# Kernel optimization log

Measured on AMD Instinct MI355X. Metric: run time of the kernel, lower is better.

The kernel has to match this reference:

```python
import jax, jax.numpy as jnp
import numpy as np

EPS = 1e-5

def _conv1x1(x, w, b):
    # x: [B, Cin, L], w: [Cout, Cin], b: [Cout]
    return jnp.einsum('oc,bcl->bol', w, x) + b[None, :, None]

def _bn(x, g, b):
    # BatchNorm1d in training mode: batch stats over (B, L), biased variance
    m = jnp.mean(x, axis=(0, 2), keepdims=True)
    v = jnp.var(x, axis=(0, 2), keepdims=True)
    return g[None, :, None] * (x - m) * jax.lax.rsqrt(v + EPS) + b[None, :, None]

def setup_inputs() -> dict:
    key = jax.random.key(0)
    ks = jax.random.split(key, 16)
    B, H, L, K = 32, 32, 32768, 7
    rel, im, out = H // 16, H // 8, H // 4          # 2, 4, 8
    cat = (1 + K) * rel                              # 16
    w = lambda k, shape: jax.random.normal(k, shape, jnp.float32) * 0.1
    return {
        'x': jax.random.normal(ks[0], (B, H, L), jnp.float32),
        'w_phi': w(ks[1], (rel, H)),  'b_phi': w(ks[2], (rel,)),
        'w_psi': w(ks[3], (rel, H)),  'b_psi': w(ks[4], (rel,)),
        'w_beta': w(ks[5], (out, H)), 'b_beta': w(ks[6], (out,)),
        'w_cw1': w(ks[7], (im, cat)), 'b_cw1': w(ks[8], (im,)),
        'w_cw2': w(ks[9], (out, im)), 'b_cw2': w(ks[10], (out,)),
        'w_out': w(ks[11], (H, out)), 'b_out': w(ks[12], (H,)),
        'g_cat': jnp.ones((cat,), jnp.float32),  'be_cat': jnp.zeros((cat,), jnp.float32),
        'g_im': jnp.ones((im,), jnp.float32),    'be_im': jnp.zeros((im,), jnp.float32),
        'g_aggr': jnp.ones((out,), jnp.float32), 'be_aggr': jnp.zeros((out,), jnp.float32),
        'g_hid': jnp.ones((H,), jnp.float32),    'be_hid': jnp.zeros((H,), jnp.float32),
        'kernel_size': 7,
    }

def reference(x, w_phi, b_phi, w_psi, b_psi, w_beta, b_beta,
              w_cw1, b_cw1, w_cw2, b_cw2, w_out, b_out,
              g_cat, be_cat, g_im, be_im, g_aggr, be_aggr, g_hid, be_hid,
              kernel_size):
    B, H, L = x.shape
    phi = _conv1x1(x, w_phi, b_phi)                       # [B, rel, L]
    psi = _conv1x1(x, w_psi, b_psi)                       # [B, rel, L]
    p = kernel_size // 2
    psi_pad = jnp.pad(psi, ((0, 0), (0, 0), (p, p)))
    # F.unfold with kernel (k,1): channel index = c*k + j -> stack kernel axis after channel
    psi_unf = jnp.stack([psi_pad[:, :, j:j + L] for j in range(kernel_size)], axis=2)
    psi_unf = psi_unf.reshape(B, psi.shape[1] * kernel_size, L)   # [B, rel*k, L]
    h = jnp.concatenate([phi, psi_unf], axis=1)           # [B, (1+k)*rel, L]
    h = jax.nn.relu(_bn(h, g_cat, be_cat))
    h = _conv1x1(h, w_cw1, b_cw1)
    h = jax.nn.relu(_bn(h, g_im, be_im))
    weight = _conv1x1(h, w_cw2, b_cw2)                    # [B, out, L]
    beta = _conv1x1(x, w_beta, b_beta)                    # [B, out, L]
    aggr = jax.nn.relu(_bn(weight * beta, g_aggr, be_aggr))
    y = x + _conv1x1(aggr, w_out, b_out)
    return jax.nn.relu(_bn(y, g_hid, be_hid))
```

## Files before the change

### kernel.cpp

```cpp
#include <hip/hip_runtime.h>
#include <math.h>

#define Bn 32
#define Hc 32
#define Ln 32768
#define RELC 2
#define IMC 4
#define OC 8
#define CATC 16
#define KS 7
#define NPOS (Bn*Ln)
#define TPB 256
#define VPT 4
#define PPB (TPB*VPT)
#define TILES (Ln/PPB)
#define NBLK (Bn*TILES)
#define NSLOT 16
#define SSTR 128
#define PCH (RELC*PPB)
#define BCH (OC*PPB)
#define XCH (Hc*PPB)

#define iS_PHI  0
#define iSS_PHI 2
#define iS_PSI  4
#define iSS_PSI 6
#define iS_T    8
#define iSS_T   12
#define iS_AP   16
#define iSS_AP  24
#define iS_Y    32
#define iSS_Y   64
#define bPF  0
#define bPFS 6
#define bQL  12
#define bQLS 18
#define NBST 24

#define FMA4(A,S,V) { A.x=fmaf((S),(V).x,A.x); A.y=fmaf((S),(V).y,A.y); A.z=fmaf((S),(V).z,A.z); A.w=fmaf((S),(V).w,A.w); }

__device__ inline float4 affrelu(float4 v, float a, float d){
    float4 r;
    r.x=fmaxf(fmaf(a,v.x,d),0.f); r.y=fmaxf(fmaf(a,v.y,d),0.f);
    r.z=fmaxf(fmaf(a,v.z,d),0.f); r.w=fmaxf(fmaf(a,v.w,d),0.f);
    return r;
}
__device__ inline double wredd(double v){
    #pragma unroll
    for (int o=32;o>0;o>>=1) v += __shfl_down(v,o,64);
    return v;
}
__device__ inline float wredf(float v){
    #pragma unroll
    for (int o=32;o>0;o>>=1) v += __shfl_down(v,o,64);
    return v;
}
__device__ inline void atomAddD(double* p, double v){ unsafeAtomicAdd(p, v); }

__device__ inline unsigned short f2b(float f){
    unsigned int u = __float_as_uint(f);
    u += 0x7FFFu + ((u>>16)&1u);
    return (unsigned short)(u>>16);
}
__device__ inline float b2f(unsigned short h){ return __uint_as_float(((unsigned int)h)<<16); }
__device__ inline ushort4 pack4r(float4 v, float4* r){
    ushort4 h;
    h.x=f2b(v.x); h.y=f2b(v.y); h.z=f2b(v.z); h.w=f2b(v.w);
    r->x=b2f(h.x); r->y=b2f(h.y); r->z=b2f(h.z); r->w=b2f(h.w);
    return h;
}
__device__ inline ushort4 pack4(float4 v){
    ushort4 h;
    h.x=f2b(v.x); h.y=f2b(v.y); h.z=f2b(v.z); h.w=f2b(v.w);
    return h;
}
__device__ inline float4 unpack4(ushort4 h){
    return make_float4(b2f(h.x),b2f(h.y),b2f(h.z),b2f(h.w));
}
typedef unsigned short us8 __attribute__((ext_vector_type(8)));
typedef float f4nt __attribute__((ext_vector_type(4)));
__device__ inline void ntstore4(float* p, float4 v){
    union { float4 a; f4nt b; } u; u.a = v;
    __builtin_nontemporal_store(u.b, (f4nt*)p);
}

template<int NCH>
__device__ void affines(const double* __restrict__ stats, const double* __restrict__ bstats,
                        const float* g_cat, const float* be_cat,
                        const float* g_im,  const float* be_im,
                        const float* g_ag,  const float* be_ag,
                        const float* g_hid, const float* be_hid,
                        double (*redS)[16], double (*redQ)[16],
                        double* bstL, float* aAll, float* dAll, int tid)
{
    if (tid < NBST) bstL[tid] = bstats[tid];
    for (int p = tid; p < NCH*16; p += TPB){
        int ch = p >> 4, s = p & 15;
        int si, qi;
        if (ch < 2)       { si = iS_PHI+ch;           qi = iSS_PHI+ch; }
        else if (ch < 16) { int cp=(ch-2)/KS;         si = iS_PSI+cp;  qi = iSS_PSI+cp; }
        else if (ch < 20) { int i=ch-16;              si = iS_T+i;     qi = iSS_T+i; }
        else if (ch < 28) { int o=ch-20;              si = iS_AP+o;    qi = iSS_AP+o; }
        else              { int h=ch-28;              si = iS_Y+h;     qi = iSS_Y+h; }
        redS[ch][s] = stats[(size_t)s*SSTR + si];
        redQ[ch][s] = stats[(size_t)s*SSTR + qi];
    }
    __syncthreads();
    if (tid < NCH){
        double S=0, SS=0;
        #pragma unroll
        for (int s=0;s<16;++s){ S += redS[tid][s]; SS += redQ[tid][s]; }
        float g, be;
        if (tid < 16){
            if (tid >= 2){
                int cp=(tid-2)/KS, j=(tid-2)%KS, d=j-KS/2;
                if (d>0) for (int i=0;i<d;++i)   { S-=bstL[bPF+cp*3+i]; SS-=bstL[bPFS+cp*3+i]; }
                if (d<0) for (int i=3+d;i<3;++i) { S-=bstL[bQL+cp*3+i]; SS-=bstL[bQLS+cp*3+i]; }
            }
            g=g_cat[tid]; be=be_cat[tid];
        } else if (tid < 20){ g=g_im[tid-16]; be=be_im[tid-16]; }
        else if (tid < 28){ g=g_ag[tid-20]; be=be_ag[tid-20]; }
        else { g=g_hid[tid-28]; be=be_hid[tid-28]; }
        const double N=(double)NPOS;
        double m=S/N, v=SS/N-m*m, inv=1.0/sqrt(v+1e-5);
        aAll[tid]=(float)(g*inv);
        dAll[tid]=be-(float)(m*inv*g);
    }
}

__global__ void __launch_bounds__(TPB) k0(const float* __restrict__ x, unsigned short* __restrict__ xC)
{
    const int r = blockIdx.x;
    const int b = r >> 5, h = r & 31;
    const float* src = x + (size_t)r*Ln;
    unsigned short* dstBase = xC + (size_t)b*TILES*XCH + (size_t)h*PPB + threadIdx.x*4;
    const float* s4 = src + threadIdx.x*4;
    #pragma unroll 4
    for (int t = 0; t < TILES; ++t){
        float4 v = *(const float4*)(s4 + (size_t)t*PPB);
        *(ushort4*)(dstBase + (size_t)t*XCH) = pack4(v);
    }
}

__global__ void __launch_bounds__(TPB) k1c(
    const unsigned short* __restrict__ xC,
    const float* __restrict__ w_phi, const float* __restrict__ b_phi,
    const float* __restrict__ w_psi, const float* __restrict__ b_psi,
    const float* __restrict__ w_beta,const float* __restrict__ b_beta,
    unsigned short* __restrict__ phiC, unsigned short* __restrict__ psiC,
    unsigned short* __restrict__ betaC,
    double* __restrict__ stats, double* __restrict__ bstats)
{
    __shared__ __align__(16) float wl[Hc*12 + 12];
    __shared__ double rbuf[4][8];
    const int tid = threadIdx.x;
    for (int i = tid; i < Hc*12; i += TPB) {
        int h = i/12, j = i%12;
        float v;
        if (j < 2)      v = w_phi[j*Hc + h];
        else if (j < 4) v = w_psi[(j-2)*Hc + h];
        else            v = w_beta[(j-4)*Hc + h];
        wl[h*12 + j] = v;
    }
    if (tid < 12)
        wl[Hc*12+tid] = (tid<2) ? b_phi[tid] : (tid<4) ? b_psi[tid-2] : b_beta[tid-4];
    __syncthreads();

    const int cidx = blockIdx.x;
    const int tile = cidx % TILES;
    const int li   = tid*VPT;
    double* st = stats + (size_t)(cidx & (NSLOT-1))*SSTR;

    float4 acc[12];
    #pragma unroll
    for (int j=0;j<12;++j){ float bb = wl[Hc*12+j]; acc[j]=make_float4(bb,bb,bb,bb); }

    const unsigned short* xb = xC + (size_t)cidx*XCH + li;
    #pragma unroll 8
    for (int h=0; h<Hc; ++h) {
        const float4 xv = unpack4(*(const ushort4*)(xb + (size_t)h*PPB));
        const float4 w0 = *(const float4*)(&wl[h*12+0]);
        const float4 w1 = *(const float4*)(&wl[h*12+4]);
        const float4 w2 = *(const float4*)(&wl[h*12+8]);
        FMA4(acc[0],w0.x,xv); FMA4(acc[1],w0.y,xv); FMA4(acc[2],w0.z,xv); FMA4(acc[3],w0.w,xv);
        FMA4(acc[4],w1.x,xv); FMA4(acc[5],w1.y,xv); FMA4(acc[6],w1.z,xv); FMA4(acc[7],w1.w,xv);
        FMA4(acc[8],w2.x,xv); FMA4(acc[9],w2.y,xv); FMA4(acc[10],w2.z,xv); FMA4(acc[11],w2.w,xv);
    }
    float4 rphi[2], rpsi[2];
    #pragma unroll
    for (int c=0;c<RELC;++c){
        ushort4 hp = pack4r(acc[c], &rphi[c]);
        *(ushort4*)(phiC + (size_t)cidx*PCH + c*PPB + li) = hp;
        ushort4 hq = pack4r(acc[2+c], &rpsi[c]);
        *(ushort4*)(psiC + (size_t)cidx*PCH + c*PPB + li) = hq;
    }
    #pragma unroll
    for (int o=0;o<OC;++o)
        *(ushort4*)(betaC + (size_t)cidx*BCH + o*PPB + li) = pack4(acc[4+o]);

    double vals[8];
    #pragma unroll
    for (int c=0;c<2;++c){
        float4 v = rphi[c];
        vals[c]   = (double)v.x+v.y+v.z+v.w;
        vals[2+c] = (double)v.x*v.x+(double)v.y*v.y+(double)v.z*v.z+(double)v.w*v.w;
        float4 u = rpsi[c];
        vals[4+c] = (double)u.x+u.y+u.z+u.w;
        vals[6+c] = (double)u.x*u.x+(double)u.y*u.y+(double)u.z*u.z+(double)u.w*u.w;
    }
    if (tile==0 || tile==TILES-1) {
        #pragma unroll
        for (int c=0;c<2;++c){
            const float pv[4] = {rpsi[c].x, rpsi[c].y, rpsi[c].z, rpsi[c].w};
            #pragma unroll
            for (int e=0;e<4;++e){
                int le = tile*PPB + li + e;
                if (le < 3) {
                    atomAddD(&bstats[bPF +c*3+le], (double)pv[e]);
                    atomAddD(&bstats[bPFS+c*3+le], (double)pv[e]*pv[e]);
                }
                if (le >= Ln-3) {
                    int i = le-(Ln-3);
                    atomAddD(&bstats[bQL +c*3+i], (double)pv[e]);
                    atomAddD(&bstats[bQLS+c*3+i], (double)pv[e]*pv[e]);
                }
            }
        }
    }
    const int lane=tid&63, wid=tid>>6;
    #pragma unroll
    for (int i=0;i<8;++i){ double r=wredd(vals[i]); if(lane==0) rbuf[wid][i]=r; }
    __syncthreads();
    if (tid<8) atomAddD(&st[iS_PHI+tid], rbuf[0][tid]+rbuf[1][tid]+rbuf[2][tid]+rbuf[3][tid]);
}

#define STAGE_PSI_V(psiT)                                                                  \
    {                                                                                      \
        int c_ = tid >> 7, k_ = tid & 127;                                                 \
        us8 v_ = *(const us8*)(psiC + (size_t)cidx*PCH + c_*PPB + 8*k_);                   \
        _Pragma("unroll")                                                                  \
        for (int j_=0;j_<8;++j_) psiT[c_][3+8*k_+j_] = b2f(v_[j_]);                        \
        if (tid < 6){ int cc=tid/3, ii=tid%3;                                              \
            psiT[cc][ii] = (tile>0) ? b2f(psiC[(size_t)(cidx-1)*PCH + cc*PPB + 1021+ii]) : 0.f; }\
        else if (tid < 12){ int kk=tid-6, cc=kk/3, ii=kk%3;                                \
            psiT[cc][1027+ii] = (tile<TILES-1) ? b2f(psiC[(size_t)(cidx+1)*PCH + cc*PPB + ii]) : 0.f; } \
    }

#define COMPUTE_T(tacc,aCat,dCat,w1s,b1s,psiT)                                             \
    _Pragma("unroll")                                                                      \
    for (int o=0;o<IMC;++o){ float bb=b1s[o]; tacc[o]=make_float4(bb,bb,bb,bb); }          \
    _Pragma("unroll")                                                                      \
    for (int c=0;c<RELC;++c){                                                              \
        float4 pv = unpack4(*(const ushort4*)(phiC + (size_t)cidx*PCH + c*PPB + li));      \
        float4 hv = affrelu(pv, aCat[c], dCat[c]);                                         \
        _Pragma("unroll")                                                                  \
        for (int o=0;o<IMC;++o) FMA4(tacc[o], w1s[o*CATC+c], hv);                          \
    }                                                                                      \
    _Pragma("unroll")                                                                      \
    for (int c=0;c<RELC;++c){                                                              \
        float4 A  = *(const float4*)&psiT[c][li];                                          \
        float4 Bv = *(const float4*)&psiT[c][li+4];                                        \
        float4 Cv = *(const float4*)&psiT[c][li+8];                                        \
        float pr[12] = {A.x,A.y,A.z,A.w, Bv.x,Bv.y,Bv.z,Bv.w, Cv.x,Cv.y,Cv.z,Cv.w};        \
        _Pragma("unroll")                                                                  \
        for (int j=0;j<KS;++j){                                                            \
            int ch = 2 + c*KS + j;                                                         \
            float a=aCat[ch], d=dCat[ch];                                                  \
            float4 hv;                                                                     \
            hv.x=fmaxf(fmaf(a,pr[j+0],d),0.f);                                             \
            hv.y=fmaxf(fmaf(a,pr[j+1],d),0.f);                                             \
            hv.z=fmaxf(fmaf(a,pr[j+2],d),0.f);                                             \
            hv.w=fmaxf(fmaf(a,pr[j+3],d),0.f);                                             \
            _Pragma("unroll")                                                              \
            for (int o=0;o<IMC;++o) FMA4(tacc[o], w1s[o*CATC+ch], hv);                     \
        }                                                                                  \
    }

#define COMPUTE_AG(ag,tacc,aIm,dIm,aAg,dAg,w2s,b2s)                                        \
    {                                                                                      \
        float4 h2[IMC];                                                                    \
        _Pragma("unroll")                                                                  \
        for (int i=0;i<IMC;++i) h2[i]=affrelu(tacc[i],aIm[i],dIm[i]);                      \
        _Pragma("unroll")                                                                  \
        for (int o=0;o<OC;++o){                                                            \
            float bb=b2s[o];                                                               \
            float4 w=make_float4(bb,bb,bb,bb);                                             \
            _Pragma("unroll")                                                              \
            for (int i=0;i<IMC;++i) FMA4(w,w2s[o*IMC+i],h2[i]);                            \
            float4 bv = unpack4(*(const ushort4*)(betaC + (size_t)cidx*BCH + o*PPB + li)); \
            float4 av; av.x=w.x*bv.x; av.y=w.y*bv.y; av.z=w.z*bv.z; av.w=w.w*bv.w;         \
            ag[o]=affrelu(av, aAg[o], dAg[o]);                                             \
        }                                                                                  \
    }

__global__ void __launch_bounds__(TPB) k3t(
    const unsigned short* __restrict__ phiC, const unsigned short* __restrict__ psiC,
    const float* __restrict__ w_cw1, const float* __restrict__ b_cw1,
    const float* __restrict__ g_cat, const float* __restrict__ be_cat,
    double* __restrict__ stats, const double* __restrict__ bstats)
{
    __shared__ float w1s[IMC*CATC], b1s[IMC];
    __shared__ __align__(16) float psiT[2][1032];
    __shared__ double rbuf[4][8];
    __shared__ double redS[16][16], redQ[16][16];
    __shared__ double bstL[NBST];
    __shared__ float aAll[16], dAll[16];
    const int tid = threadIdx.x;
    const int cidx = blockIdx.x;
    const int tile = cidx % TILES;
    const int li   = tid*VPT;
    double* st = stats + (size_t)(cidx & (NSLOT-1))*SSTR;

    if (tid < IMC*CATC) w1s[tid] = w_cw1[tid];
    if (tid < IMC)      b1s[tid] = b_cw1[tid];
    STAGE_PSI_V(psiT)
    affines<16>(stats,bstats, g_cat,be_cat, 0,0, 0,0, 0,0, redS,redQ,bstL,aAll,dAll, tid);
    __syncthreads();

    float4 tacc[IMC];
    COMPUTE_T(tacc,aAll,dAll,w1s,b1s,psiT)

    double vals[8];
    #pragma unroll
    for (int o=0;o<IMC;++o){
        float4 v = tacc[o];
        vals[o]   = (double)v.x+v.y+v.z+v.w;
        vals[4+o] = (double)v.x*v.x+(double)v.y*v.y+(double)v.z*v.z+(double)v.w*v.w;
    }
    const int lane=tid&63, wid=tid>>6;
    #pragma unroll
    for (int i=0;i<8;++i){ double r=wredd(vals[i]); if(lane==0) rbuf[wid][i]=r; }
    __syncthreads();
    if (tid<8) atomAddD(&st[iS_T+tid], rbuf[0][tid]+rbuf[1][tid]+rbuf[2][tid]+rbuf[3][tid]);
}

__global__ void __launch_bounds__(TPB) k5a(
    const unsigned short* __restrict__ phiC, const unsigned short* __restrict__ psiC,
    const unsigned short* __restrict__ betaC,
    const float* __restrict__ w_cw1, const float* __restrict__ b_cw1,
    const float* __restrict__ w_cw2, const float* __restrict__ b_cw2,
    const float* __restrict__ g_cat, const float* __restrict__ be_cat,
    const float* __restrict__ g_im,  const float* __restrict__ be_im,
    double* __restrict__ stats, const double* __restrict__ bstats)
{
    __shared__ float w1s[IMC*CATC], b1s[IMC], w2s[OC*IMC], b2s[OC];
    __shared__ __align__(16) float psiT[2][1032];
    __shared__ double rbuf[4][16];
    __shared__ double redS[20][16], redQ[20][16];
    __shared__ double bstL[NBST];
    __shared__ float aAll[20], dAll[20];
    const int tid = threadIdx.x;
    const int cidx = blockIdx.x;
    const int tile = cidx % TILES;
    const int li   = tid*VPT;
    double* st = stats + (size_t)(cidx & (NSLOT-1))*SSTR;

    if (tid < IMC*CATC) w1s[tid] = w_cw1[tid];
    if (tid < IMC)      b1s[tid] = b_cw1[tid];
    if (tid>=64 && tid<64+OC*IMC) w2s[tid-64]=w_cw2[tid-64];
    if (tid>=96 && tid<96+OC)     b2s[tid-96]=b_cw2[tid-96];
    STAGE_PSI_V(psiT)
    affines<20>(stats,bstats, g_cat,be_cat, g_im,be_im, 0,0, 0,0, redS,redQ,bstL,aAll,dAll, tid);
    __syncthreads();

    float4 tacc[IMC];
    COMPUTE_T(tacc,aAll,dAll,w1s,b1s,psiT)

    double vals[16];
    {
        float4 h2[IMC];
        #pragma unroll
        for (int i=0;i<IMC;++i) h2[i]=affrelu(tacc[i],aAll[16+i],dAll[16+i]);
        #pragma unroll
        for (int o=0;o<OC;++o){
            float bb=b2s[o];
            float4 w=make_float4(bb,bb,bb,bb);
            #pragma unroll
            for (int i=0;i<IMC;++i) FMA4(w,w2s[o*IMC+i],h2[i]);
            float4 bv = unpack4(*(const ushort4*)(betaC + (size_t)cidx*BCH + o*PPB + li));
            float4 av; av.x=w.x*bv.x; av.y=w.y*bv.y; av.z=w.z*bv.z; av.w=w.w*bv.w;
            vals[o]   = (double)av.x+av.y+av.z+av.w;
            vals[8+o] = (double)av.x*av.x+(double)av.y*av.y+(double)av.z*av.z+(double)av.w*av.w;
        }
    }
    const int lane=tid&63, wid=tid>>6;
    #pragma unroll
    for (int i=0;i<16;++i){ double r=wredd(vals[i]); if(lane==0) rbuf[wid][i]=r; }
    __syncthreads();
    if (tid<16) atomAddD(&st[iS_AP+tid], rbuf[0][tid]+rbuf[1][tid]+rbuf[2][tid]+rbuf[3][tid]);
}

__global__ void __launch_bounds__(TPB) k7y(
    const unsigned short* __restrict__ xC,
    const unsigned short* __restrict__ phiC, const unsigned short* __restrict__ psiC,
    const unsigned short* __restrict__ betaC,
    const float* __restrict__ w_cw1, const float* __restrict__ b_cw1,
    const float* __restrict__ w_cw2, const float* __restrict__ b_cw2,
    const float* __restrict__ w_out, const float* __restrict__ b_out,
    const float* __restrict__ g_cat, const float* __restrict__ be_cat,
    const float* __restrict__ g_im,  const float* __restrict__ be_im,
    const float* __restrict__ g_ag,  const float* __restrict__ be_ag,
    double* __restrict__ stats, const double* __restrict__ bstats)
{
    __shared__ float w1s[IMC*CATC], b1s[IMC], w2s[OC*IMC], b2s[OC];
    __shared__ __align__(16) float wos[Hc*OC];
    __shared__ float bos[Hc];
    __shared__ __align__(16) float psiT[2][1032];
    __shared__ float fredS[Hc][4], fredQ[Hc][4];
    __shared__ double redS[28][16], redQ[28][16];
    __shared__ double bstL[NBST];
    __shared__ float aAll[28], dAll[28];
    const int tid = threadIdx.x;
    const int cidx = blockIdx.x;
    const int tile = cidx % TILES;
    const int li   = tid*VPT;
    double* st = stats + (size_t)(cidx & (NSLOT-1))*SSTR;

    if (tid < IMC*CATC) w1s[tid] = w_cw1[tid];
    if (tid < IMC)      b1s[tid] = b_cw1[tid];
    if (tid>=64 && tid<64+OC*IMC) w2s[tid-64]=w_cw2[tid-64];
    if (tid>=96 && tid<96+OC)     b2s[tid-96]=b_cw2[tid-96];
    wos[tid] = w_out[tid];
    if (tid>=128 && tid<128+Hc) bos[tid-128]=b_out[tid-128];
    STAGE_PSI_V(psiT)
    affines<28>(stats,bstats, g_cat,be_cat, g_im,be_im, g_ag,be_ag, 0,0,
                redS,redQ,bstL,aAll,dAll, tid);
    __syncthreads();

    float4 tacc[IMC];
    COMPUTE_T(tacc,aAll,dAll,w1s,b1s,psiT)
    float4 ag[OC];
    COMPUTE_AG(ag,tacc,(aAll+16),(dAll+16),(aAll+20),(dAll+20),w2s,b2s)

    const int lane=tid&63, wid=tid>>6;
    const unsigned short* xb = xC + (size_t)cidx*XCH + li;
    #pragma unroll 8
    for (int h=0;h<Hc;++h){
        float4 y = unpack4(*(const ushort4*)(xb + (size_t)h*PPB));
        float bb=bos[h]; y.x+=bb; y.y+=bb; y.z+=bb; y.w+=bb;
        #pragma unroll
        for (int o=0;o<OC;++o) FMA4(y, wos[h*OC+o], ag[o]);
        float fs=y.x+y.y+y.z+y.w;
        float fq=y.x*y.x+y.y*y.y+y.z*y.z+y.w*y.w;
        fs=wredf(fs); fq=wredf(fq);
        if (lane==0){ fredS[h][wid]=fs; fredQ[h][wid]=fq; }
    }
    __syncthreads();
    if (tid<Hc){
        double s=(double)fredS[tid][0]+fredS[tid][1]+fredS[tid][2]+fredS[tid][3];
        double q=(double)fredQ[tid][0]+fredQ[tid][1]+fredQ[tid][2]+fredQ[tid][3];
        atomAddD(&st[iS_Y +tid], s);
        atomAddD(&st[iSS_Y+tid], q);
    }
}

__global__ void __launch_bounds__(TPB) k9o(
    const unsigned short* __restrict__ xC,
    const unsigned short* __restrict__ phiC, const unsigned short* __restrict__ psiC,
    const unsigned short* __restrict__ betaC,
    const float* __restrict__ w_cw1, const float* __restrict__ b_cw1,
    const float* __restrict__ w_cw2, const float* __restrict__ b_cw2,
    const float* __restrict__ w_out, const float* __restrict__ b_out,
    const float* __restrict__ g_cat, const float* __restrict__ be_cat,
    const float* __restrict__ g_im,  const float* __restrict__ be_im,
    const float* __restrict__ g_ag,  const float* __restrict__ be_ag,
    const float* __restrict__ g_hid, const float* __restrict__ be_hid,
    float* __restrict__ out,
    const double* __restrict__ stats, const double* __restrict__ bstats)
{
    __shared__ float w1s[IMC*CATC], b1s[IMC], w2s[OC*IMC], b2s[OC];
    __shared__ __align__(16) float wos[Hc*OC];
    __shared__ float bos[Hc];
    __shared__ __align__(16) float psiT[2][1032];
    __shared__ double redS[60][16], redQ[60][16];
    __shared__ double bstL[NBST];
    __shared__ float aAll[60], dAll[60];
    const int tid = threadIdx.x;
    const int cidx = blockIdx.x;
    const int b    = cidx / TILES;
    const int tile = cidx % TILES;
    const int li   = tid*VPT;

    if (tid < IMC*CATC) w1s[tid] = w_cw1[tid];
    if (tid < IMC)      b1s[tid] = b_cw1[tid];
    if (tid>=64 && tid<64+OC*IMC) w2s[tid-64]=w_cw2[tid-64];
    if (tid>=96 && tid<96+OC)     b2s[tid-96]=b_cw2[tid-96];
    wos[tid] = w_out[tid];
    if (tid>=128 && tid<128+Hc) bos[tid-128]=b_out[tid-128];
    STAGE_PSI_V(psiT)
    affines<60>(stats,bstats, g_cat,be_cat, g_im,be_im, g_ag,be_ag, g_hid,be_hid,
                redS,redQ,bstL,aAll,dAll, tid);
    __syncthreads();

    float4 tacc[IMC];
    COMPUTE_T(tacc,aAll,dAll,w1s,b1s,psiT)
    float4 ag[OC];
    COMPUTE_AG(ag,tacc,(aAll+16),(dAll+16),(aAll+20),(dAll+20),w2s,b2s)

    const unsigned short* xb = xC + (size_t)cidx*XCH + li;
    float* ob = out + (size_t)b*Hc*Ln + (size_t)tile*PPB + li;
    #pragma unroll 8
    for (int h=0;h<Hc;++h){
        float4 y = unpack4(*(const ushort4*)(xb + (size_t)h*PPB));
        float bb=bos[h]; y.x+=bb; y.y+=bb; y.z+=bb; y.w+=bb;
        #pragma unroll
        for (int o=0;o<OC;++o) FMA4(y, wos[h*OC+o], ag[o]);
        ntstore4(ob + (size_t)h*Ln, affrelu(y, aAll[28+h], dAll[28+h]));
    }
}

extern "C" void kernel_launch(void* const* d_in, const int* in_sizes, int n_in,
                              void* d_out, int out_size, void* d_ws, size_t ws_size,
                              hipStream_t stream)
{
    const float* x     =(const float*)d_in[0];
    const float* w_phi =(const float*)d_in[1];  const float* b_phi =(const float*)d_in[2];
    const float* w_psi =(const float*)d_in[3];  const float* b_psi =(const float*)d_in[4];
    const float* w_beta=(const float*)d_in[5];  const float* b_beta=(const float*)d_in[6];
    const float* w_cw1 =(const float*)d_in[7];  const float* b_cw1 =(const float*)d_in[8];
    const float* w_cw2 =(const float*)d_in[9];  const float* b_cw2 =(const float*)d_in[10];
    const float* w_out =(const float*)d_in[11]; const float* b_out =(const float*)d_in[12];
    const float* g_cat =(const float*)d_in[13]; const float* be_cat=(const float*)d_in[14];
    const float* g_im  =(const float*)d_in[15]; const float* be_im =(const float*)d_in[16];
    const float* g_ag  =(const float*)d_in[17]; const float* be_ag =(const float*)d_in[18];
    const float* g_hid =(const float*)d_in[19]; const float* be_hid=(const float*)d_in[20];

    double* stats  = (double*)d_ws;
    double* bstats = stats + (size_t)NSLOT*SSTR;
    unsigned short* base = (unsigned short*)((char*)d_ws + 32768);
    unsigned short* phiC  = base;
    unsigned short* psiC  = phiC  + (size_t)NBLK*PCH;
    unsigned short* betaC = psiC  + (size_t)NBLK*PCH;
    unsigned short* xC    = betaC + (size_t)NBLK*BCH;

    hipMemsetAsync(d_ws, 0, ((size_t)NSLOT*SSTR + NBST)*sizeof(double), stream);
    k0 <<<Bn*Hc, TPB, 0, stream>>>(x, xC);
    k1c<<<NBLK, TPB, 0, stream>>>(xC, w_phi,b_phi, w_psi,b_psi, w_beta,b_beta,
                                  phiC,psiC,betaC, stats,bstats);
    k3t<<<NBLK, TPB, 0, stream>>>(phiC,psiC, w_cw1,b_cw1, g_cat,be_cat, stats,bstats);
    k5a<<<NBLK, TPB, 0, stream>>>(phiC,psiC,betaC, w_cw1,b_cw1, w_cw2,b_cw2,
                                  g_cat,be_cat, g_im,be_im, stats,bstats);
    k7y<<<NBLK, TPB, 0, stream>>>(xC, phiC,psiC,betaC, w_cw1,b_cw1, w_cw2,b_cw2, w_out,b_out,
                                  g_cat,be_cat, g_im,be_im, g_ag,be_ag, stats,bstats);
    k9o<<<NBLK, TPB, 0, stream>>>(xC, phiC,psiC,betaC, w_cw1,b_cw1, w_cw2,b_cw2, w_out,b_out,
                                  g_cat,be_cat, g_im,be_im, g_ag,be_ag, g_hid,be_hid,
                                  (float*)d_out, stats,bstats);
}
```

Measured before the change: 167.3 us.

## Materialize aggregated activations in k7y and slim final kernel to read them

k7y now writes the post-BN aggregated activations (rounded to 16-bit) to a new workspace buffer. The final kernel reads them back instead of recomputing psi staging, the cw1/cw2 convolutions and the BN affines, so it only has to finalize the hidden BN stats. The x-channel loops in k1c, k7y and k9s are also restructured to issue 8 loads before consuming them, giving more memory-level parallelism. In exchange this adds an extra write and read of the ag tensor, and k7y now uses the rounded ag values for its stats so they match what the final kernel sees.

```diff
diff --git a/kernel.cpp b/kernel.cpp
--- a/kernel.cpp
+++ b/kernel.cpp
@@ -176,15 +176,22 @@
     for (int j=0;j<12;++j){ float bb = wl[Hc*12+j]; acc[j]=make_float4(bb,bb,bb,bb); }
 
     const unsigned short* xb = xC + (size_t)cidx*XCH + li;
-    #pragma unroll 8
-    for (int h=0; h<Hc; ++h) {
-        const float4 xv = unpack4(*(const ushort4*)(xb + (size_t)h*PPB));
-        const float4 w0 = *(const float4*)(&wl[h*12+0]);
-        const float4 w1 = *(const float4*)(&wl[h*12+4]);
-        const float4 w2 = *(const float4*)(&wl[h*12+8]);
-        FMA4(acc[0],w0.x,xv); FMA4(acc[1],w0.y,xv); FMA4(acc[2],w0.z,xv); FMA4(acc[3],w0.w,xv);
-        FMA4(acc[4],w1.x,xv); FMA4(acc[5],w1.y,xv); FMA4(acc[6],w1.z,xv); FMA4(acc[7],w1.w,xv);
-        FMA4(acc[8],w2.x,xv); FMA4(acc[9],w2.y,xv); FMA4(acc[10],w2.z,xv); FMA4(acc[11],w2.w,xv);
+    #pragma unroll
+    for (int g=0; g<4; ++g){
+        ushort4 xv[8];
+        #pragma unroll
+        for (int j=0;j<8;++j) xv[j] = *(const ushort4*)(xb + (size_t)(g*8+j)*PPB);
+        #pragma unroll
+        for (int j=0;j<8;++j){
+            const int h = g*8+j;
+            const float4 x4 = unpack4(xv[j]);
+            const float4 w0 = *(const float4*)(&wl[h*12+0]);
+            const float4 w1 = *(const float4*)(&wl[h*12+4]);
+            const float4 w2 = *(const float4*)(&wl[h*12+8]);
+            FMA4(acc[0],w0.x,x4); FMA4(acc[1],w0.y,x4); FMA4(acc[2],w0.z,x4); FMA4(acc[3],w0.w,x4);
+            FMA4(acc[4],w1.x,x4); FMA4(acc[5],w1.y,x4); FMA4(acc[6],w1.z,x4); FMA4(acc[7],w1.w,x4);
+            FMA4(acc[8],w2.x,x4); FMA4(acc[9],w2.y,x4); FMA4(acc[10],w2.z,x4); FMA4(acc[11],w2.w,x4);
+        }
     }
     float4 rphi[2], rpsi[2];
     #pragma unroll
@@ -393,7 +400,7 @@
 __global__ void __launch_bounds__(TPB) k7y(
     const unsigned short* __restrict__ xC,
     const unsigned short* __restrict__ phiC, const unsigned short* __restrict__ psiC,
-    const unsigned short* __restrict__ betaC,
+    const unsigned short* __restrict__ betaC, unsigned short* __restrict__ agC,
     const float* __restrict__ w_cw1, const float* __restrict__ b_cw1,
     const float* __restrict__ w_cw2, const float* __restrict__ b_cw2,
     const float* __restrict__ w_out, const float* __restrict__ b_out,
@@ -431,19 +438,31 @@
     COMPUTE_T(tacc,aAll,dAll,w1s,b1s,psiT)
     float4 ag[OC];
     COMPUTE_AG(ag,tacc,(aAll+16),(dAll+16),(aAll+20),(dAll+20),w2s,b2s)
+    #pragma unroll
+    for (int o=0;o<OC;++o){
+        ushort4 hh = pack4r(ag[o], &ag[o]);
+        *(ushort4*)(agC + (size_t)cidx*BCH + o*PPB + li) = hh;
+    }
 
     const int lane=tid&63, wid=tid>>6;
     const unsigned short* xb = xC + (size_t)cidx*XCH + li;
-    #pragma unroll 8
-    for (int h=0;h<Hc;++h){
-        float4 y = unpack4(*(const ushort4*)(xb + (size_t)h*PPB));
-        float bb=bos[h]; y.x+=bb; y.y+=bb; y.z+=bb; y.w+=bb;
-        #pragma unroll
-        for (int o=0;o<OC;++o) FMA4(y, wos[h*OC+o], ag[o]);
-        float fs=y.x+y.y+y.z+y.w;
-        float fq=y.x*y.x+y.y*y.y+y.z*y.z+y.w*y.w;
-        fs=wredf(fs); fq=wredf(fq);
-        if (lane==0){ fredS[h][wid]=fs; fredQ[h][wid]=fq; }
+    #pragma unroll
+    for (int g=0; g<4; ++g){
+        ushort4 xv[8];
+        #pragma unroll
+        for (int j=0;j<8;++j) xv[j] = *(const ushort4*)(xb + (size_t)(g*8+j)*PPB);
+        #pragma unroll
+        for (int j=0;j<8;++j){
+            const int h = g*8+j;
+            float4 y = unpack4(xv[j]);
+            float bb=bos[h]; y.x+=bb; y.y+=bb; y.z+=bb; y.w+=bb;
+            #pragma unroll
+            for (int o=0;o<OC;++o) FMA4(y, wos[h*OC+o], ag[o]);
+            float fs=y.x+y.y+y.z+y.w;
+            float fq=y.x*y.x+y.y*y.y+y.z*y.z+y.w*y.w;
+            fs=wredf(fs); fq=wredf(fq);
+            if (lane==0){ fredS[h][wid]=fs; fredQ[h][wid]=fq; }
+        }
     }
     __syncthreads();
     if (tid<Hc){
@@ -454,58 +473,65 @@
     }
 }
 
-__global__ void __launch_bounds__(TPB) k9o(
-    const unsigned short* __restrict__ xC,
-    const unsigned short* __restrict__ phiC, const unsigned short* __restrict__ psiC,
-    const unsigned short* __restrict__ betaC,
-    const float* __restrict__ w_cw1, const float* __restrict__ b_cw1,
-    const float* __restrict__ w_cw2, const float* __restrict__ b_cw2,
+__global__ void __launch_bounds__(TPB) k9s(
+    const unsigned short* __restrict__ xC, const unsigned short* __restrict__ agC,
     const float* __restrict__ w_out, const float* __restrict__ b_out,
-    const float* __restrict__ g_cat, const float* __restrict__ be_cat,
-    const float* __restrict__ g_im,  const float* __restrict__ be_im,
-    const float* __restrict__ g_ag,  const float* __restrict__ be_ag,
     const float* __restrict__ g_hid, const float* __restrict__ be_hid,
-    float* __restrict__ out,
-    const double* __restrict__ stats, const double* __restrict__ bstats)
-{
-    __shared__ float w1s[IMC*CATC], b1s[IMC], w2s[OC*IMC], b2s[OC];
+    float* __restrict__ out, const double* __restrict__ stats)
+{
+    __shared__ double redS[Hc][16], redQ[Hc][16];
+    __shared__ float aH[Hc], dH[Hc];
     __shared__ __align__(16) float wos[Hc*OC];
     __shared__ float bos[Hc];
-    __shared__ __align__(16) float psiT[2][1032];
-    __shared__ double redS[60][16], redQ[60][16];
-    __shared__ double bstL[NBST];
-    __shared__ float aAll[60], dAll[60];
     const int tid = threadIdx.x;
     const int cidx = blockIdx.x;
     const int b    = cidx / TILES;
     const int tile = cidx % TILES;
     const int li   = tid*VPT;
 
-    if (tid < IMC*CATC) w1s[tid] = w_cw1[tid];
-    if (tid < IMC)      b1s[tid] = b_cw1[tid];
-    if (tid>=64 && tid<64+OC*IMC) w2s[tid-64]=w_cw2[tid-64];
-    if (tid>=96 && tid<96+OC)     b2s[tid-96]=b_cw2[tid-96];
     wos[tid] = w_out[tid];
     if (tid>=128 && tid<128+Hc) bos[tid-128]=b_out[tid-128];
-    STAGE_PSI_V(psiT)
-    affines<60>(stats,bstats, g_cat,be_cat, g_im,be_im, g_ag,be_ag, g_hid,be_hid,
-                redS,redQ,bstL,aAll,dAll, tid);
-    __syncthreads();
-
-    float4 tacc[IMC];
-    COMPUTE_T(tacc,aAll,dAll,w1s,b1s,psiT)
+    for (int p = tid; p < Hc*16; p += TPB){
+        int ch = p >> 4, s = p & 15;
+        redS[ch][s] = stats[(size_t)s*SSTR + iS_Y + ch];
+        redQ[ch][s] = stats[(size_t)s*SSTR + iSS_Y + ch];
+    }
+    __syncthreads();
+    if (tid < Hc){
+        double S=0, SS=0;
+        #pragma unroll
+        for (int s=0;s<16;++s){ S += redS[tid][s]; SS += redQ[tid][s]; }
+        const double N=(double)NPOS;
+        double m=S/N, v=SS/N-m*m, inv=1.0/sqrt(v+1e-5);
+        aH[tid]=(float)(g_hid[tid]*inv);
+        dH[tid]=be_hid[tid]-(float)(m*inv*g_hid[tid]);
+    }
+    __syncthreads();
+
     float4 ag[OC];
-    COMPUTE_AG(ag,tacc,(aAll+16),(dAll+16),(aAll+20),(dAll+20),w2s,b2s)
-
+    {
+        ushort4 av[OC];
+        #pragma unroll
+        for (int o=0;o<OC;++o) av[o] = *(const ushort4*)(agC + (size_t)cidx*BCH + o*PPB + li);
+        #pragma unroll
+        for (int o=0;o<OC;++o) ag[o] = unpack4(av[o]);
+    }
     const unsigned short* xb = xC + (size_t)cidx*XCH + li;
     float* ob = out + (size_t)b*Hc*Ln + (size_t)tile*PPB + li;
-    #pragma unroll 8
-    for (int h=0;h<Hc;++h){
-        float4 y = unpack4(*(const ushort4*)(xb + (size_t)h*PPB));
-        float bb=bos[h]; y.x+=bb; y.y+=bb; y.z+=bb; y.w+=bb;
-        #pragma unroll
-        for (int o=0;o<OC;++o) FMA4(y, wos[h*OC+o], ag[o]);
-        ntstore4(ob + (size_t)h*Ln, affrelu(y, aAll[28+h], dAll[28+h]));
+    #pragma unroll
+    for (int g=0; g<4; ++g){
+        ushort4 xv[8];
+        #pragma unroll
+        for (int j=0;j<8;++j) xv[j] = *(const ushort4*)(xb + (size_t)(g*8+j)*PPB);
+        #pragma unroll
+        for (int j=0;j<8;++j){
+            const int h = g*8+j;
+            float4 y = unpack4(xv[j]);
+            float bb=bos[h]; y.x+=bb; y.y+=bb; y.z+=bb; y.w+=bb;
+            #pragma unroll
+            for (int o=0;o<OC;++o) FMA4(y, wos[h*OC+o], ag[o]);
+            ntstore4(ob + (size_t)h*Ln, affrelu(y, aH[h], dH[h]));
+        }
     }
 }
 
@@ -532,6 +558,7 @@
     unsigned short* psiC  = phiC  + (size_t)NBLK*PCH;
     unsigned short* betaC = psiC  + (size_t)NBLK*PCH;
     unsigned short* xC    = betaC + (size_t)NBLK*BCH;
+    unsigned short* agC   = xC    + (size_t)NBLK*XCH;
 
     hipMemsetAsync(d_ws, 0, ((size_t)NSLOT*SSTR + NBST)*sizeof(double), stream);
     k0 <<<Bn*Hc, TPB, 0, stream>>>(x, xC);
@@ -540,9 +567,9 @@
     k3t<<<NBLK, TPB, 0, stream>>>(phiC,psiC, w_cw1,b_cw1, g_cat,be_cat, stats,bstats);
     k5a<<<NBLK, TPB, 0, stream>>>(phiC,psiC,betaC, w_cw1,b_cw1, w_cw2,b_cw2,
                                   g_cat,be_cat, g_im,be_im, stats,bstats);
-    k7y<<<NBLK, TPB, 0, stream>>>(xC, phiC,psiC,betaC, w_cw1,b_cw1, w_cw2,b_cw2, w_out,b_out,
-                                  g_cat,be_cat, g_im,be_im, g_ag,be_ag, stats,bstats);
-    k9o<<<NBLK, TPB, 0, stream>>>(xC, phiC,psiC,betaC, w_cw1,b_cw1, w_cw2,b_cw2, w_out,b_out,
-                                  g_cat,be_cat, g_im,be_im, g_ag,be_ag, g_hid,be_hid,
-                                  (float*)d_out, stats,bstats);
-}
+    k7y<<<NBLK, TPB, 0, stream>>>(xC, phiC,psiC,betaC, agC, w_cw1,b_cw1, w_cw2,b_cw2,
+                                  w_out,b_out, g_cat,be_cat, g_im,be_im, g_ag,be_ag,
+                                  stats,bstats);
+    k9s<<<NBLK, TPB, 0, stream>>>(xC, agC, w_out,b_out, g_hid,be_hid,
+                                  (float*)d_out, stats);
+}
```

After: 166.9 us. Within noise of the previous version (-0.3%).
